# Performance work log

Hardware: AMD Instinct MI355X
Metric: run time of the kernel (lower is better)

Reference implementation:

```python
import jax, jax.numpy as jnp
import numpy as np

SEQ, B, NIN, NHID = 512, 64, 1024, 1024

def setup_inputs() -> dict:
    key = jax.random.key(0)
    k1, k2, k3 = jax.random.split(key, 3)
    x = jax.random.normal(k1, (SEQ, B, NIN), dtype=jnp.float32)
    # nn.Linear(ninput+nhid, 4*nhid): weight (4*nhid, ninput+nhid), bias (4*nhid,)
    bound = 1.0 / np.sqrt(NIN + NHID)
    W = jax.random.uniform(k2, (4 * NHID, NIN + NHID), dtype=jnp.float32, minval=-bound, maxval=bound)
    b = jax.random.uniform(k3, (4 * NHID,), dtype=jnp.float32, minval=-bound, maxval=bound)
    return {"x": x, "W": W, "b": b}

def reference(x, W, b):
    nhid = W.shape[0] // 4
    batch = x.shape[1]
    # split weight: columns [0:NIN] act on x_t, [NIN:] act on h
    def step(carry, x_t):
        h, c = carry
        a = jnp.concatenate([x_t, h], axis=1) @ W.T + b  # (B, 4*nhid)
        i = jax.nn.sigmoid(a[:, :nhid])
        f = jax.nn.sigmoid(a[:, nhid:2 * nhid])
        o = jax.nn.sigmoid(a[:, 2 * nhid:3 * nhid])
        g = jnp.tanh(a[:, 3 * nhid:])
        c = c * f + i * g
        h = o * jnp.tanh(c)
        return (h, c), h
    h0 = jnp.zeros((batch, nhid), dtype=x.dtype)
    c0 = jnp.zeros((batch, nhid), dtype=x.dtype)
    (h, c), output = jax.lax.scan(step, (h0, c0), x)
    return (output, h)
```

## Files before the change

kernel.cpp:

```cpp
#include <hip/hip_runtime.h>
#include <hip/hip_bf16.h>
#include <stdint.h>
#include <stddef.h>

#define SEQ   512
#define BATCH 64
#define NIN   1024
#define NHID  1024
#define NG    4096

typedef __attribute__((ext_vector_type(8))) short bf16x8;
typedef __attribute__((ext_vector_type(4))) float f32x4;
typedef __attribute__((ext_vector_type(4))) uint32_t u32x4;

static __device__ __forceinline__ ushort f2bf(float f) {
  uint32_t u = __builtin_bit_cast(uint32_t, f);
  uint32_t lsb = (u >> 16) & 1u;
  u += 0x7fffu + lsb;
  return (ushort)(u >> 16);
}

static __device__ __forceinline__ f32x4 mfma_bf16(bf16x8 a, bf16x8 b, f32x4 c) {
  return __builtin_amdgcn_mfma_f32_16x16x32_bf16(a, b, c, 0, 0, 0);
}

static __device__ __forceinline__ void lds_load16(const ushort* g, ushort* l) {
  __builtin_amdgcn_global_load_lds(
      (const __attribute__((address_space(1))) void*)g,
      (__attribute__((address_space(3))) void*)l, 16, 0, 0);
}

static __device__ __forceinline__ void st_short_dev(ushort* p, uint32_t v) {
  asm volatile("global_store_short %0, %1, off sc1" :: "v"(p), "v"(v) : "memory");
}
static __device__ __forceinline__ void st_dword_dev(uint32_t* p, uint32_t v) {
  asm volatile("global_store_dword %0, %1, off sc1" :: "v"(p), "v"(v) : "memory");
}
static __device__ __forceinline__ void st_x4_dev(ushort* p, u32x4 v) {
  asm volatile("global_store_dwordx4 %0, %1, off sc1" :: "v"(p), "v"(v) : "memory");
}
static __device__ __forceinline__ uint32_t ld_dword_dev(const uint32_t* p) {
  uint32_t v;
  asm volatile("global_load_dword %0, %1, off sc1" : "=v"(v) : "v"(p) : "memory");
  return v;
}
static __device__ __forceinline__ u32x4 ld_x4_dev(const ushort* p) {
  u32x4 v;
  asm volatile("global_load_dwordx4 %0, %1, off sc1" : "=v"(v) : "v"(p) : "memory");
  return v;
}

#define WAITV(n) do { asm volatile("s_waitcnt vmcnt(" #n ")" ::: "memory"); \
                      __builtin_amdgcn_sched_barrier(0); } while (0)

static __device__ __forceinline__ float sigm_f(float x) {
  return __builtin_amdgcn_rcpf(1.f + __expf(-x));
}
static __device__ __forceinline__ float tanh_f(float x) {
  return 1.f - 2.f * __builtin_amdgcn_rcpf(__expf(2.f * x) + 1.f);
}


__global__ __launch_bounds__(256) void k_convert_x(const float* __restrict__ X,
                                                   ushort* __restrict__ Xb, int n4) {
  int i = blockIdx.x * 256 + threadIdx.x;
  if (i < n4) {
    float4 v = ((const float4*)X)[i];
    ushort4 o;
    o.x = f2bf(v.x); o.y = f2bf(v.y); o.z = f2bf(v.z); o.w = f2bf(v.w);
    ((ushort4*)Xb)[i] = o;
  }
}

__global__ __launch_bounds__(256) void k_convert_w(const float* __restrict__ W,
                                                   const float* __restrict__ bvec,
                                                   ushort* __restrict__ Wxb,
                                                   ushort* __restrict__ Whb,
                                                   float* __restrict__ bp) {
  int p = blockIdx.x;
  int cg = p >> 6, g = (p >> 4) & 3, j = p & 15;
  int r = g * 1024 + cg * 16 + j;
  const float* src = W + (size_t)r * 2048;
  for (int k4 = threadIdx.x; k4 < 512; k4 += 256) {
    float4 v = ((const float4*)src)[k4];
    ushort4 o;
    o.x = f2bf(v.x); o.y = f2bf(v.y); o.z = f2bf(v.z); o.w = f2bf(v.w);
    if (k4 < 256) ((ushort4*)(Wxb + (size_t)p * 1024))[k4] = o;
    else          ((ushort4*)(Whb + (size_t)p * 1024))[k4 - 256] = o;
  }
  if (threadIdx.x == 0) bp[p] = bvec[r];
}

__global__ __launch_bounds__(256) void k_zero(ushort* __restrict__ hb0,
                                              ushort* __restrict__ hb1,
                                              float* __restrict__ cst,
                                              uint32_t* __restrict__ flg2) {
  int i = blockIdx.x * 256 + threadIdx.x;
  st_short_dev(hb0 + i, 0u);
  st_short_dev(hb1 + i, 0u);
  cst[i] = 0.f;
  if (i < 256 * 64) st_dword_dev(flg2 + i, 0u);
}


__global__ __launch_bounds__(256) void k_gemm1(const ushort* __restrict__ Xbc,
                                               const ushort* __restrict__ Wxb,
                                               const float* __restrict__ bp,
                                               float* __restrict__ Axc) {
  __shared__ ushort As[128 * 32];
  __shared__ ushort Bs[128 * 32];
  const int m0 = blockIdx.x * 128;
  const int n0 = blockIdx.y * 128;
  const int tid = threadIdx.x;
  const int w = tid >> 6, l = tid & 63;
  const int wr = w >> 1, wc = w & 1;
  const int lr = l >> 2;
  const int lc = (l & 3) * 8;
  const int fr = l & 15, fk8 = (l >> 4) * 8, fq = l >> 4;

  f32x4 acc[4][4] = {};

  for (int kb = 0; kb < 1024; kb += 32) {
    lds_load16(Xbc + (size_t)(m0 + w * 16 + lr) * 1024 + kb + lc,       &As[w * 512]);
    lds_load16(Xbc + (size_t)(m0 + (w + 4) * 16 + lr) * 1024 + kb + lc, &As[(w + 4) * 512]);
    lds_load16(Wxb + (size_t)(n0 + w * 16 + lr) * 1024 + kb + lc,       &Bs[w * 512]);
    lds_load16(Wxb + (size_t)(n0 + (w + 4) * 16 + lr) * 1024 + kb + lc, &Bs[(w + 4) * 512]);
    __syncthreads();
    bf16x8 af[4], bfr[4];
#pragma unroll
    for (int i = 0; i < 4; i++) af[i]  = *(const bf16x8*)&As[(wr * 64 + i * 16 + fr) * 32 + fk8];
#pragma unroll
    for (int i = 0; i < 4; i++) bfr[i] = *(const bf16x8*)&Bs[(wc * 64 + i * 16 + fr) * 32 + fk8];
#pragma unroll
    for (int i = 0; i < 4; i++)
#pragma unroll
      for (int jj = 0; jj < 4; jj++)
        acc[i][jj] = mfma_bf16(af[i], bfr[jj], acc[i][jj]);
    __syncthreads();
  }

#pragma unroll
  for (int jj = 0; jj < 4; jj++) {
    int gc = n0 + wc * 64 + jj * 16 + fr;
    float bb = bp[gc];
#pragma unroll
    for (int i = 0; i < 4; i++) {
      int grb = m0 + wr * 64 + i * 16 + fq * 4;
#pragma unroll
      for (int jr = 0; jr < 4; jr++)
        Axc[(size_t)(grb + jr) * NG + gc] = acc[i][jj][jr] + bb;
    }
  }
}


__global__ __launch_bounds__(256) void k_persist(const ushort* __restrict__ Whb,
                                                 const float* __restrict__ Axc,
                                                 ushort* __restrict__ hb0,
                                                 ushort* __restrict__ hb1,
                                                 float* __restrict__ out,
                                                 uint32_t* __restrict__ flg2,
                                                 float* __restrict__ cst,
                                                 int t0, int TC) {
  __shared__ ushort Wlds[8192 * 8];
  __shared__ float red[4][16][65];
  __shared__ ushort h_sh[16][16];

  const int bid = blockIdx.x;
  const int team = bid >> 6, hg = bid & 63;
  const int tid = threadIdx.x, w = tid >> 6, l = tid & 63;
  const int fr = l & 15, fq = l >> 4;

  for (int it = 0; it < 32; ++it) {
    int f = it * 256 + tid;
    int fl = f & 63, bj = (f >> 6) & 3, kc = f >> 8;
    bf16x8 v = *(const bf16x8*)(Whb + (size_t)(hg * 64 + bj * 16 + (fl & 15)) * 1024
                                + kc * 32 + (fl >> 4) * 8);
    *(bf16x8*)&Wlds[(size_t)f * 8] = v;
  }
  __syncthreads();

  const int eb = tid >> 4, ej = tid & 15;
  const int hidx_self = (team * 16 + eb) * 1024 + hg * 16 + ej;
  float creg = cst[hidx_self];

  const size_t roff = (size_t)(team * 16 + fr) * 1024 + w * 256 + fq * 8;
  const uint32_t* fladdr = flg2 + bid * 64 + l;

  for (int tt = 0; tt < TC; ++tt) {
    const int t = t0 + tt;
    const ushort* hb_r = (t & 1) ? hb0 : hb1;
    ushort*       hb_w = (t & 1) ? hb1 : hb0;

    const float* axp = Axc + ((size_t)tt * 64 + team * 16 + eb) * NG + hg * 64;
    float ax0 = axp[ej], ax1 = axp[16 + ej], ax2 = axp[32 + ej], ax3 = axp[48 + ej];

    if (t > 0) {
      int guard = 0;
      while (true) {
        uint32_t v = ld_dword_dev(fladdr);
        WAITV(0);
        if (__all((int)(v >= (uint32_t)t))) break;
        if (++guard > (1 << 15)) break;
      }
    }

    const ushort* aBt = hb_r + roff;
    u32x4 hv[8];
    f32x4 acc[4] = {};
#pragma unroll
    for (int ks = 0; ks < 8; ++ks) hv[ks] = ld_x4_dev(aBt + ks * 32);
#define SLICE(ks) do {                                                        \
      bf16x8 a_ = __builtin_bit_cast(bf16x8, hv[ks]);                         \
      _Pragma("unroll")                                                       \
      for (int bj = 0; bj < 4; ++bj) {                                        \
        bf16x8 b_ = *(const bf16x8*)&Wlds[(size_t)(((w * 8 + (ks)) * 4 + bj) * 64 + l) * 8]; \
        acc[bj] = mfma_bf16(a_, b_, acc[bj]);                                 \
      }                                                                       \
    } while (0)
    WAITV(7); SLICE(0);
    WAITV(6); SLICE(1);
    WAITV(5); SLICE(2);
    WAITV(4); SLICE(3);
    WAITV(3); SLICE(4);
    WAITV(2); SLICE(5);
    WAITV(1); SLICE(6);
    WAITV(0); SLICE(7);
#undef SLICE

#pragma unroll
    for (int bj = 0; bj < 4; ++bj)
#pragma unroll
      for (int jr = 0; jr < 4; ++jr)
        red[w][fq * 4 + jr][bj * 16 + fr] = acc[bj][jr];
    __syncthreads();

    float ai_ = 0.f, af_ = 0.f, ao_ = 0.f, ag_ = 0.f;
#pragma unroll
    for (int ww = 0; ww < 4; ++ww) {
      ai_ += red[ww][eb][ej];
      af_ += red[ww][eb][16 + ej];
      ao_ += red[ww][eb][32 + ej];
      ag_ += red[ww][eb][48 + ej];
    }
    ai_ += ax0; af_ += ax1; ao_ += ax2; ag_ += ax3;

    float ig = sigm_f(ai_);
    float fg = sigm_f(af_);
    float og = sigm_f(ao_);
    float gg = tanh_f(ag_);
    creg = creg * fg + ig * gg;
    float h = og * tanh_f(creg);
    h_sh[eb][ej] = f2bf(h);
    __syncthreads();

    if (w == 0) {
      if (l < 32) {
        int prow = l >> 1, phalf = (l & 1) * 8;
        u32x4 pv = *(const u32x4*)&h_sh[prow][phalf];
        st_x4_dev(hb_w + (size_t)(team * 16 + prow) * 1024 + hg * 16 + phalf, pv);
      }
      asm volatile("s_waitcnt vmcnt(0)" ::: "memory");
      __builtin_amdgcn_sched_barrier(0);
      st_dword_dev(flg2 + (team * 64 + l) * 64 + hg, (uint32_t)(t + 1));
    }

    out[(size_t)t * 65536 + hidx_self] = h;
    if (t == SEQ - 1) out[(size_t)SEQ * 65536 + hidx_self] = h;
  }

  cst[hidx_self] = creg;
}


__global__ __launch_bounds__(256) void k_step(int t,
                                              const ushort* __restrict__ Xb,
                                              const ushort* __restrict__ Wxb,
                                              const ushort* __restrict__ Whb,
                                              const float* __restrict__ bp,
                                              const ushort* __restrict__ hprev,
                                              ushort* __restrict__ hnext,
                                              float* __restrict__ cst,
                                              float* __restrict__ out) {
  __shared__ float red[4][16][65];
  const int bidx = blockIdx.x;
  const int cg = bidx & 63, mb = bidx >> 6;
  const int b0 = mb * 16, pcol = cg * 64;
  const int tid = threadIdx.x, w = tid >> 6, l = tid & 63;
  const int fr = l & 15, fk8 = (l >> 4) * 8, fq = l >> 4;

  f32x4 acc[4] = {};

  const ushort* aSrc;
  const ushort* bMat;
  int kbase;
  if (w < 2) { aSrc = Xb + (size_t)(t * 64 + b0 + fr) * 1024 + w * 512 + fk8; bMat = Wxb; kbase = w * 512; }
  else       { aSrc = hprev + (size_t)(b0 + fr) * 1024 + (w - 2) * 512 + fk8; bMat = Whb; kbase = (w - 2) * 512; }
  const ushort* bRow = bMat + (size_t)(pcol + fr) * 1024 + kbase + fk8;

#pragma unroll
  for (int ks = 0; ks < 16; ks++) {
    int kk = ks * 32;
    bf16x8 a = *(const bf16x8*)(aSrc + kk);
#pragma unroll
    for (int bj = 0; bj < 4; bj++) {
      bf16x8 bfv = *(const bf16x8*)(bRow + (size_t)bj * 16 * 1024 + kk);
      acc[bj] = mfma_bf16(a, bfv, acc[bj]);
    }
  }

#pragma unroll
  for (int bj = 0; bj < 4; bj++)
#pragma unroll
    for (int jr = 0; jr < 4; jr++)
      red[w][fq * 4 + jr][bj * 16 + fr] = acc[bj][jr];
  __syncthreads();

  const int b = tid >> 4, j = tid & 15;
  float ai_ = 0.f, af_ = 0.f, ao_ = 0.f, ag_ = 0.f;
#pragma unroll
  for (int ww = 0; ww < 4; ww++) {
    ai_ += red[ww][b][j];
    af_ += red[ww][b][16 + j];
    ao_ += red[ww][b][32 + j];
    ag_ += red[ww][b][48 + j];
  }
  ai_ += bp[pcol + j]; af_ += bp[pcol + 16 + j]; ao_ += bp[pcol + 32 + j]; ag_ += bp[pcol + 48 + j];

  float ig = sigm_f(ai_);
  float fg = sigm_f(af_);
  float og = sigm_f(ao_);
  float gg = tanh_f(ag_);
  int hidx = (b0 + b) * 1024 + cg * 16 + j;
  float cn = cst[hidx] * fg + ig * gg;
  cst[hidx] = cn;
  float h = og * tanh_f(cn);
  out[(size_t)t * 65536 + hidx] = h;
  hnext[hidx] = f2bf(h);
  if (t == SEQ - 1) out[(size_t)SEQ * 65536 + hidx] = h;
}


extern "C" void kernel_launch(void* const* d_in, const int* in_sizes, int n_in,
                              void* d_out, int out_size, void* d_ws, size_t ws_size,
                              hipStream_t stream) {
  const float* X    = (const float*)d_in[0];
  const float* W    = (const float*)d_in[1];
  const float* bvec = (const float*)d_in[2];
  float* out = (float*)d_out;
  char* ws = (char*)d_ws;

  size_t off = 0;
  auto alloc = [&](size_t bytes) -> char* {
    char* p = ws + off;
    off += (bytes + 255) & ~(size_t)255;
    return p;
  };
  ushort*   Xb   = (ushort*)alloc((size_t)SEQ * BATCH * NIN * 2);
  ushort*   Wxb  = (ushort*)alloc((size_t)NG * NIN * 2);
  ushort*   Whb  = (ushort*)alloc((size_t)NG * NHID * 2);
  float*    bp   = (float*)alloc((size_t)NG * 4);
  ushort*   hb0  = (ushort*)alloc((size_t)BATCH * NHID * 2);
  ushort*   hb1  = (ushort*)alloc((size_t)BATCH * NHID * 2);
  float*    cst  = (float*)alloc((size_t)BATCH * NHID * 4);
  uint32_t* flg2 = (uint32_t*)alloc(256 * 64 * 4);
  size_t base_need = off;

  if (ws_size < base_need) return;

  size_t avail = ws_size - base_need;
  int TC = 0;
  for (int tc = 512; tc >= 16; tc >>= 1) {
    if ((size_t)tc * 64 * NG * 4 <= avail) { TC = tc; break; }
  }
  float* Axc = (float*)(ws + base_need);

  k_convert_x<<<(SEQ * BATCH * NIN / 4 + 255) / 256, 256, 0, stream>>>(X, Xb, SEQ * BATCH * NIN / 4);
  k_convert_w<<<NG, 256, 0, stream>>>(W, bvec, Wxb, Whb, bp);
  k_zero<<<BATCH * NHID / 256, 256, 0, stream>>>(hb0, hb1, cst, flg2);

  if (TC > 0) {
    for (int c = 0; c < SEQ / TC; ++c) {
      k_gemm1<<<dim3(TC * 64 / 128, NG / 128), 256, 0, stream>>>(
          Xb + (size_t)c * TC * 64 * 1024, Wxb, bp, Axc);
      k_persist<<<256, 256, 0, stream>>>(Whb, Axc, hb0, hb1, out, flg2, cst, c * TC, TC);
    }
  } else {
    for (int t = 0; t < SEQ; t++) {
      const ushort* hp = (t & 1) ? hb1 : hb0;
      ushort*       hn = (t & 1) ? hb0 : hb1;
      k_step<<<256, 256, 0, stream>>>(t, Xb, Wxb, Whb, bp, hp, hn, cst, out);
    }
  }
}
```

Measured before the change: 2.296 ms.

## Fuse input projection into persistent LSTM kernel, split waves between x and h

```diff
diff --git a/kernel.cpp b/kernel.cpp
--- a/kernel.cpp
+++ b/kernel.cpp
@@ -22,12 +22,6 @@
 
 static __device__ __forceinline__ f32x4 mfma_bf16(bf16x8 a, bf16x8 b, f32x4 c) {
   return __builtin_amdgcn_mfma_f32_16x16x32_bf16(a, b, c, 0, 0, 0);
-}
-
-static __device__ __forceinline__ void lds_load16(const ushort* g, ushort* l) {
-  __builtin_amdgcn_global_load_lds(
-      (const __attribute__((address_space(1))) void*)g,
-      (__attribute__((address_space(3))) void*)l, 16, 0, 0);
 }
 
 static __device__ __forceinline__ void st_short_dev(ushort* p, uint32_t v) {
@@ -103,65 +97,15 @@
 }
 
 
-__global__ __launch_bounds__(256) void k_gemm1(const ushort* __restrict__ Xbc,
-                                               const ushort* __restrict__ Wxb,
-                                               const float* __restrict__ bp,
-                                               float* __restrict__ Axc) {
-  __shared__ ushort As[128 * 32];
-  __shared__ ushort Bs[128 * 32];
-  const int m0 = blockIdx.x * 128;
-  const int n0 = blockIdx.y * 128;
-  const int tid = threadIdx.x;
-  const int w = tid >> 6, l = tid & 63;
-  const int wr = w >> 1, wc = w & 1;
-  const int lr = l >> 2;
-  const int lc = (l & 3) * 8;
-  const int fr = l & 15, fk8 = (l >> 4) * 8, fq = l >> 4;
-
-  f32x4 acc[4][4] = {};
-
-  for (int kb = 0; kb < 1024; kb += 32) {
-    lds_load16(Xbc + (size_t)(m0 + w * 16 + lr) * 1024 + kb + lc,       &As[w * 512]);
-    lds_load16(Xbc + (size_t)(m0 + (w + 4) * 16 + lr) * 1024 + kb + lc, &As[(w + 4) * 512]);
-    lds_load16(Wxb + (size_t)(n0 + w * 16 + lr) * 1024 + kb + lc,       &Bs[w * 512]);
-    lds_load16(Wxb + (size_t)(n0 + (w + 4) * 16 + lr) * 1024 + kb + lc, &Bs[(w + 4) * 512]);
-    __syncthreads();
-    bf16x8 af[4], bfr[4];
-#pragma unroll
-    for (int i = 0; i < 4; i++) af[i]  = *(const bf16x8*)&As[(wr * 64 + i * 16 + fr) * 32 + fk8];
-#pragma unroll
-    for (int i = 0; i < 4; i++) bfr[i] = *(const bf16x8*)&Bs[(wc * 64 + i * 16 + fr) * 32 + fk8];
-#pragma unroll
-    for (int i = 0; i < 4; i++)
-#pragma unroll
-      for (int jj = 0; jj < 4; jj++)
-        acc[i][jj] = mfma_bf16(af[i], bfr[jj], acc[i][jj]);
-    __syncthreads();
-  }
-
-#pragma unroll
-  for (int jj = 0; jj < 4; jj++) {
-    int gc = n0 + wc * 64 + jj * 16 + fr;
-    float bb = bp[gc];
-#pragma unroll
-    for (int i = 0; i < 4; i++) {
-      int grb = m0 + wr * 64 + i * 16 + fq * 4;
-#pragma unroll
-      for (int jr = 0; jr < 4; jr++)
-        Axc[(size_t)(grb + jr) * NG + gc] = acc[i][jj][jr] + bb;
-    }
-  }
-}
-
-
 __global__ __launch_bounds__(256) void k_persist(const ushort* __restrict__ Whb,
-                                                 const float* __restrict__ Axc,
+                                                 const ushort* __restrict__ Wxb,
+                                                 const ushort* __restrict__ Xb,
+                                                 const float* __restrict__ bp,
                                                  ushort* __restrict__ hb0,
                                                  ushort* __restrict__ hb1,
                                                  float* __restrict__ out,
                                                  uint32_t* __restrict__ flg2,
-                                                 float* __restrict__ cst,
-                                                 int t0, int TC) {
+                                                 float* __restrict__ cst) {
   __shared__ ushort Wlds[8192 * 8];
   __shared__ float red[4][16][65];
   __shared__ ushort h_sh[16][16];
@@ -183,50 +127,71 @@
   const int eb = tid >> 4, ej = tid & 15;
   const int hidx_self = (team * 16 + eb) * 1024 + hg * 16 + ej;
   float creg = cst[hidx_self];
-
-  const size_t roff = (size_t)(team * 16 + fr) * 1024 + w * 256 + fq * 8;
-  const uint32_t* fladdr = flg2 + bid * 64 + l;
-
-  for (int tt = 0; tt < TC; ++tt) {
-    const int t = t0 + tt;
+  const int pcol = hg * 64;
+  const float bpc0 = bp[pcol + ej],      bpc1 = bp[pcol + 16 + ej];
+  const float bpc2 = bp[pcol + 32 + ej], bpc3 = bp[pcol + 48 + ej];
+
+  for (int t = 0; t < SEQ; ++t) {
     const ushort* hb_r = (t & 1) ? hb0 : hb1;
     ushort*       hb_w = (t & 1) ? hb1 : hb0;
 
-    const float* axp = Axc + ((size_t)tt * 64 + team * 16 + eb) * NG + hg * 64;
-    float ax0 = axp[ej], ax1 = axp[16 + ej], ax2 = axp[32 + ej], ax3 = axp[48 + ej];
-
-    if (t > 0) {
-      int guard = 0;
-      while (true) {
-        uint32_t v = ld_dword_dev(fladdr);
-        WAITV(0);
-        if (__all((int)(v >= (uint32_t)t))) break;
-        if (++guard > (1 << 15)) break;
+    f32x4 acc[4] = {};
+
+    if (w < 2) {
+      const ushort* ax_ = Xb + ((size_t)t * 64 + team * 16 + fr) * 1024 + w * 512 + fq * 8;
+      const ushort* bx_ = Wxb + (size_t)(hg * 64 + fr) * 1024 + w * 512 + fq * 8;
+#pragma unroll
+      for (int ks = 0; ks < 16; ++ks) {
+        bf16x8 a_ = *(const bf16x8*)(ax_ + ks * 32);
+#pragma unroll
+        for (int bj = 0; bj < 4; ++bj) {
+          bf16x8 b_ = *(const bf16x8*)(bx_ + (size_t)bj * 16 * 1024 + ks * 32);
+          acc[bj] = mfma_bf16(a_, b_, acc[bj]);
+        }
       }
-    }
-
-    const ushort* aBt = hb_r + roff;
-    u32x4 hv[8];
-    f32x4 acc[4] = {};
-#pragma unroll
-    for (int ks = 0; ks < 8; ++ks) hv[ks] = ld_x4_dev(aBt + ks * 32);
+    } else {
+      const uint32_t* fl_ = flg2 + bid * 64 + (w - 2) * 32 + (l & 31);
+      if (t > 0) {
+        int guard = 0;
+        while (true) {
+          uint32_t v = ld_dword_dev(fl_);
+          WAITV(0);
+          if (__all((int)(v >= (uint32_t)t))) break;
+          if (++guard > (1 << 15)) break;
+        }
+      }
+      const ushort* aBt = hb_r + (size_t)(team * 16 + fr) * 1024
+                          + (size_t)(w - 2) * 512 + fq * 8;
+      u32x4 hv[16];
+#pragma unroll
+      for (int ks = 0; ks < 16; ++ks) hv[ks] = ld_x4_dev(aBt + ks * 32);
+      const int kc0 = (w - 2) * 16;
 #define SLICE(ks) do {                                                        \
       bf16x8 a_ = __builtin_bit_cast(bf16x8, hv[ks]);                         \
       _Pragma("unroll")                                                       \
       for (int bj = 0; bj < 4; ++bj) {                                        \
-        bf16x8 b_ = *(const bf16x8*)&Wlds[(size_t)(((w * 8 + (ks)) * 4 + bj) * 64 + l) * 8]; \
+        bf16x8 b_ = *(const bf16x8*)&Wlds[(size_t)(((kc0 + (ks)) * 4 + bj) * 64 + l) * 8]; \
         acc[bj] = mfma_bf16(a_, b_, acc[bj]);                                 \
       }                                                                       \
     } while (0)
-    WAITV(7); SLICE(0);
-    WAITV(6); SLICE(1);
-    WAITV(5); SLICE(2);
-    WAITV(4); SLICE(3);
-    WAITV(3); SLICE(4);
-    WAITV(2); SLICE(5);
-    WAITV(1); SLICE(6);
-    WAITV(0); SLICE(7);
+      WAITV(15); SLICE(0);
+      WAITV(14); SLICE(1);
+      WAITV(13); SLICE(2);
+      WAITV(12); SLICE(3);
+      WAITV(11); SLICE(4);
+      WAITV(10); SLICE(5);
+      WAITV(9);  SLICE(6);
+      WAITV(8);  SLICE(7);
+      WAITV(7);  SLICE(8);
+      WAITV(6);  SLICE(9);
+      WAITV(5);  SLICE(10);
+      WAITV(4);  SLICE(11);
+      WAITV(3);  SLICE(12);
+      WAITV(2);  SLICE(13);
+      WAITV(1);  SLICE(14);
+      WAITV(0);  SLICE(15);
 #undef SLICE
+    }
 
 #pragma unroll
     for (int bj = 0; bj < 4; ++bj)
@@ -235,7 +200,7 @@
         red[w][fq * 4 + jr][bj * 16 + fr] = acc[bj][jr];
     __syncthreads();
 
-    float ai_ = 0.f, af_ = 0.f, ao_ = 0.f, ag_ = 0.f;
+    float ai_ = bpc0, af_ = bpc1, ao_ = bpc2, ag_ = bpc3;
 #pragma unroll
     for (int ww = 0; ww < 4; ++ww) {
       ai_ += red[ww][eb][ej];
@@ -243,7 +208,6 @@
       ao_ += red[ww][eb][32 + ej];
       ag_ += red[ww][eb][48 + ej];
     }
-    ai_ += ax0; af_ += ax1; ao_ += ax2; ag_ += ax3;
 
     float ig = sigm_f(ai_);
     float fg = sigm_f(af_);
@@ -270,74 +234,6 @@
   }
 
   cst[hidx_self] = creg;
-}
-
-
-__global__ __launch_bounds__(256) void k_step(int t,
-                                              const ushort* __restrict__ Xb,
-                                              const ushort* __restrict__ Wxb,
-                                              const ushort* __restrict__ Whb,
-                                              const float* __restrict__ bp,
-                                              const ushort* __restrict__ hprev,
-                                              ushort* __restrict__ hnext,
-                                              float* __restrict__ cst,
-                                              float* __restrict__ out) {
-  __shared__ float red[4][16][65];
-  const int bidx = blockIdx.x;
-  const int cg = bidx & 63, mb = bidx >> 6;
-  const int b0 = mb * 16, pcol = cg * 64;
-  const int tid = threadIdx.x, w = tid >> 6, l = tid & 63;
-  const int fr = l & 15, fk8 = (l >> 4) * 8, fq = l >> 4;
-
-  f32x4 acc[4] = {};
-
-  const ushort* aSrc;
-  const ushort* bMat;
-  int kbase;
-  if (w < 2) { aSrc = Xb + (size_t)(t * 64 + b0 + fr) * 1024 + w * 512 + fk8; bMat = Wxb; kbase = w * 512; }
-  else       { aSrc = hprev + (size_t)(b0 + fr) * 1024 + (w - 2) * 512 + fk8; bMat = Whb; kbase = (w - 2) * 512; }
-  const ushort* bRow = bMat + (size_t)(pcol + fr) * 1024 + kbase + fk8;
-
-#pragma unroll
-  for (int ks = 0; ks < 16; ks++) {
-    int kk = ks * 32;
-    bf16x8 a = *(const bf16x8*)(aSrc + kk);
-#pragma unroll
-    for (int bj = 0; bj < 4; bj++) {
-      bf16x8 bfv = *(const bf16x8*)(bRow + (size_t)bj * 16 * 1024 + kk);
-      acc[bj] = mfma_bf16(a, bfv, acc[bj]);
-    }
-  }
-
-#pragma unroll
-  for (int bj = 0; bj < 4; bj++)
-#pragma unroll
-    for (int jr = 0; jr < 4; jr++)
-      red[w][fq * 4 + jr][bj * 16 + fr] = acc[bj][jr];
-  __syncthreads();
-
-  const int b = tid >> 4, j = tid & 15;
-  float ai_ = 0.f, af_ = 0.f, ao_ = 0.f, ag_ = 0.f;
-#pragma unroll
-  for (int ww = 0; ww < 4; ww++) {
-    ai_ += red[ww][b][j];
-    af_ += red[ww][b][16 + j];
-    ao_ += red[ww][b][32 + j];
-    ag_ += red[ww][b][48 + j];
-  }
-  ai_ += bp[pcol + j]; af_ += bp[pcol + 16 + j]; ao_ += bp[pcol + 32 + j]; ag_ += bp[pcol + 48 + j];
-
-  float ig = sigm_f(ai_);
-  float fg = sigm_f(af_);
-  float og = sigm_f(ao_);
-  float gg = tanh_f(ag_);
-  int hidx = (b0 + b) * 1024 + cg * 16 + j;
-  float cn = cst[hidx] * fg + ig * gg;
-  cst[hidx] = cn;
-  float h = og * tanh_f(cn);
-  out[(size_t)t * 65536 + hidx] = h;
-  hnext[hidx] = f2bf(h);
-  if (t == SEQ - 1) out[(size_t)SEQ * 65536 + hidx] = h;
 }
 
 
@@ -368,28 +264,9 @@
 
   if (ws_size < base_need) return;
 
-  size_t avail = ws_size - base_need;
-  int TC = 0;
-  for (int tc = 512; tc >= 16; tc >>= 1) {
-    if ((size_t)tc * 64 * NG * 4 <= avail) { TC = tc; break; }
-  }
-  float* Axc = (float*)(ws + base_need);
-
   k_convert_x<<<(SEQ * BATCH * NIN / 4 + 255) / 256, 256, 0, stream>>>(X, Xb, SEQ * BATCH * NIN / 4);
   k_convert_w<<<NG, 256, 0, stream>>>(W, bvec, Wxb, Whb, bp);
   k_zero<<<BATCH * NHID / 256, 256, 0, stream>>>(hb0, hb1, cst, flg2);
 
-  if (TC > 0) {
-    for (int c = 0; c < SEQ / TC; ++c) {
-      k_gemm1<<<dim3(TC * 64 / 128, NG / 128), 256, 0, stream>>>(
-          Xb + (size_t)c * TC * 64 * 1024, Wxb, bp, Axc);
-      k_persist<<<256, 256, 0, stream>>>(Whb, Axc, hb0, hb1, out, flg2, cst, c * TC, TC);
-    }
-  } else {
-    for (int t = 0; t < SEQ; t++) {
-      const ushort* hp = (t & 1) ? hb1 : hb0;
-      ushort*       hn = (t & 1) ? hb0 : hb1;
-      k_step<<<256, 256, 0, stream>>>(t, Xb, Wxb, Whb, bp, hp, hn, cst, out);
-    }
-  }
-}
+  k_persist<<<256, 256, 0, stream>>>(Whb, Wxb, Xb, bp, hb0, hb1, out, flg2, cst);
+}
```

Result: slower. 4.029 ms (+75.5%).
